# Performance work log

Measured on AMD Instinct MI355X. Metric: run time of the kernel, lower is better.

The kernel has to match this reference:

```python
import jax, jax.numpy as jnp
import numpy as np

L = 4        # num_blocks
D = 512      # d_model
H = 8        # num_heads
DFF = 2048   # d_ff
EPS = 1.1920929e-07  # torch RMSNorm default eps = finfo(fp32).eps


def setup_inputs() -> dict:
    key = jax.random.key(0)
    ks = jax.random.split(key, 12)
    B, S = 4, 1024
    s = 0.02
    return {
        "x": jax.random.normal(ks[0], (B, S, D), jnp.float32),
        "col_ids": jax.random.randint(ks[1], (B, S), 0, 32),
        "row_ids": jax.random.randint(ks[2], (B, S), 0, 128),
        "nbr_ids": jax.random.randint(ks[3], (B, S), 0, 64),
        # per-block, per-relation attention weights (nn.Linear: y = x @ W.T)
        "Wq": jax.random.normal(ks[4], (L, 4, D, D), jnp.float32) * s,
        "Wk": jax.random.normal(ks[5], (L, 4, D, D), jnp.float32) * s,
        "Wv": jax.random.normal(ks[6], (L, 4, D, D), jnp.float32) * s,
        "Wo": jax.random.normal(ks[7], (L, 4, D, D), jnp.float32) * s,
        # SwiGLU FFN weights per block
        "W1": jax.random.normal(ks[8], (L, DFF, D), jnp.float32) * s,
        "W3": jax.random.normal(ks[9], (L, DFF, D), jnp.float32) * s,
        "W2": jax.random.normal(ks[10], (L, D, DFF), jnp.float32) * s,
        # RMSNorm scales: 4 attn norms + 1 ffn norm per block + final norm_out
        "g_attn": jnp.ones((L, 4, D), jnp.float32),
        "g_ffn": jnp.ones((L, D), jnp.float32),
        "g_out": jnp.ones((D,), jnp.float32),
    }


def _rms(x, g):
    return x * jax.lax.rsqrt(jnp.mean(x * x, axis=-1, keepdims=True) + EPS) * g


def _attn(x, wq, wk, wv, wo, mask):
    # x: [B,S,D]; mask: [B,S,S] bool (True = attend) or None for full attention
    B, S, _ = x.shape
    hd = D // H
    scale = 1.0 / np.sqrt(hd).astype(np.float32)
    q = (x @ wq.T).reshape(B, S, H, hd).transpose(0, 2, 1, 3)  # bhsd
    k = (x @ wk.T).reshape(B, S, H, hd).transpose(0, 2, 1, 3)
    v = (x @ wv.T).reshape(B, S, H, hd).transpose(0, 2, 1, 3)
    sc = jnp.einsum('bhqd,bhkd->bhqk', q, k) * scale
    if mask is not None:
        sc = jnp.where(mask[:, None, :, :], sc, jnp.float32(-1e30))
    a = jax.nn.softmax(sc, axis=-1)
    o = jnp.einsum('bhqk,bhkd->bhqd', a, v).transpose(0, 2, 1, 3).reshape(B, S, D)
    return o @ wo.T


def reference(x, col_ids, row_ids, nbr_ids, Wq, Wk, Wv, Wo, W1, W3, W2, g_attn, g_ffn, g_out):
    # relation order in RelationalBlock: col, feat, nbr, full
    masks = [ids[:, :, None] == ids[:, None, :] for ids in (col_ids, row_ids, nbr_ids)] + [None]
    for l in range(L):
        for r in range(4):
            x = x + _attn(_rms(x, g_attn[l, r]), Wq[l, r], Wk[l, r], Wv[l, r], Wo[l, r], masks[r])
        h = _rms(x, g_ffn[l])
        x = x + (jax.nn.silu(h @ W1[l].T) * (h @ W3[l].T)) @ W2[l].T
    return _rms(x, g_out)
```

## Files before the change

kernel.cpp:

```cpp
#include <hip/hip_runtime.h>
#include <hip/hip_bf16.h>


typedef __attribute__((ext_vector_type(4))) float f32x4;
typedef __attribute__((ext_vector_type(8))) short s16x8;
typedef __attribute__((ext_vector_type(4))) short s16x4;

#define SEQ 1024
#define DM 512
#define MTOT 4096
#define EPSV 1.1920929e-07f
#define LOG2E 1.44269504088896f

static __device__ __forceinline__ float b2f(short s) {
  unsigned u = ((unsigned)(unsigned short)s) << 16;
  return __builtin_bit_cast(float, u);
}
static __device__ __forceinline__ short f2b(float f) {
  unsigned u = __builtin_bit_cast(unsigned, f);
  u = (u + 0x7fffu + ((u >> 16) & 1u)) >> 16;
  return (short)(unsigned short)u;
}

#define MFMA_BF16(a, b, c) __builtin_amdgcn_mfma_f32_16x16x32_bf16((a), (b), (c), 0, 0, 0)
#define GLLDS(gp, lp)                                                                        \
  __builtin_amdgcn_global_load_lds((const __attribute__((address_space(1))) unsigned*)(gp),  \
                                   (__attribute__((address_space(3))) unsigned*)(lp), 16, 0, 0)
#define GLLDS4(gp, lp)                                                                       \
  __builtin_amdgcn_global_load_lds((const __attribute__((address_space(1))) unsigned*)(gp),  \
                                   (__attribute__((address_space(3))) unsigned*)(lp), 4, 0, 0)

__global__ void cvt_place(const f32x4* __restrict__ src, s16x4* __restrict__ dst, int n4,
                          int shift, int stride4, int off4, float scale) {
  int i = blockIdx.x * 256 + threadIdx.x;
  if (i >= n4) return;
  f32x4 v = src[i];
  s16x4 o;
  o[0] = f2b(v[0] * scale); o[1] = f2b(v[1] * scale);
  o[2] = f2b(v[2] * scale); o[3] = f2b(v[3] * scale);
  int c = i >> shift, r = i & ((1 << shift) - 1);
  dst[(size_t)c * stride4 + off4 + r] = o;
}

__global__ void cvt_w13(const f32x4* __restrict__ src, s16x4* __restrict__ dst, int n4, int off) {
  int i = blockIdx.x * 256 + threadIdx.x;
  if (i >= n4) return;
  f32x4 v = src[i];
  s16x4 o;
  o[0] = f2b(v[0]); o[1] = f2b(v[1]); o[2] = f2b(v[2]); o[3] = f2b(v[3]);
  int srcrow = i >> 7, r = i & 127;
  int l = srcrow >> 11, n = srcrow & 2047;
  int dstrow = l * 4096 + n * 2 + off;
  dst[(size_t)dstrow * 128 + r] = o;
}

template<bool F32OUT>
__global__ void rmsnorm_kernel(const float* __restrict__ x, const float* __restrict__ g,
                               void* __restrict__ outp) {
  int row = blockIdx.x * 4 + (threadIdx.x >> 6);
  int lane = threadIdx.x & 63;
  const float* xr = x + (size_t)row * DM + lane * 8;
  f32x4 a = *(const f32x4*)xr;
  f32x4 b = *(const f32x4*)(xr + 4);
  float ss = a[0]*a[0]+a[1]*a[1]+a[2]*a[2]+a[3]*a[3]+b[0]*b[0]+b[1]*b[1]+b[2]*b[2]+b[3]*b[3];
#pragma unroll
  for (int m = 1; m < 64; m <<= 1) ss += __shfl_xor(ss, m, 64);
  float sc = rsqrtf(ss * (1.0f / DM) + EPSV);
  const float* gp = g + lane * 8;
  if (F32OUT) {
    float* o = (float*)outp + (size_t)row * DM + lane * 8;
    f32x4 o0, o1;
#pragma unroll
    for (int j = 0; j < 4; j++) { o0[j] = a[j] * sc * gp[j]; o1[j] = b[j] * sc * gp[4 + j]; }
    *(f32x4*)o = o0;
    *(f32x4*)(o + 4) = o1;
  } else {
    s16x8 o;
#pragma unroll
    for (int j = 0; j < 4; j++) { o[j] = f2b(a[j] * sc * gp[j]); o[4 + j] = f2b(b[j] * sc * gp[4 + j]); }
    *(s16x8*)((short*)outp + (size_t)row * DM + lane * 8) = o;
  }
}

template<int AR, int AC, int FUSE>
__global__ __launch_bounds__(256) void gemm_bt(const short* __restrict__ A, const short* __restrict__ W,
                                               short* __restrict__ outb, float* __restrict__ outf,
                                               short* __restrict__ vtb, int N, int K) {
  constexpr int BM = AR * 32;
  constexpr int BN = AC * 32;
  constexpr int LPS = BM / 64 + BN / 64;
  __shared__ short As[2][BM * 32];
  __shared__ short Bs[2][BN * 32];
  const int tid = threadIdx.x;
  const int lane = tid & 63;
  const int w = tid >> 6;
  const int wr = w >> 1, wc = w & 1;
  const int m0 = blockIdx.x * BM, n0 = blockIdx.y * BN;
  f32x4 acc[AR][AC] = {};

#define STAGE_GEMM(buf, kk)                                                                      \
  {                                                                                              \
    _Pragma("unroll")                                                                            \
    for (int i = 0; i < BM / 64; i++) {                                                          \
      int s = i * 256 + tid;                                                                     \
      int row = s >> 2, gl = s & 3, gd = gl ^ ((row >> 1) & 3);                                  \
      GLLDS(A + (size_t)(m0 + row) * K + (kk) + gd * 8, (char*)As[buf] + (i * 256 + w * 64) * 16);\
    }                                                                                            \
    _Pragma("unroll")                                                                            \
    for (int i = 0; i < BN / 64; i++) {                                                          \
      int s = i * 256 + tid;                                                                     \
      int row = s >> 2, gl = s & 3, gd = gl ^ ((row >> 1) & 3);                                  \
      GLLDS(W + (size_t)(n0 + row) * K + (kk) + gd * 8, (char*)Bs[buf] + (i * 256 + w * 64) * 16);\
    }                                                                                            \
  }

  STAGE_GEMM(0, 0);
  STAGE_GEMM(1, 32);
  asm volatile("s_waitcnt vmcnt(%0)" :: "n"(LPS) : "memory");
  __builtin_amdgcn_s_barrier();
  int cur = 0;
  const int nt = K >> 5;
  for (int t = 0; t < nt; ++t) {
    s16x8 af[AR], bf[AC];
#pragma unroll
    for (int i = 0; i < AR; i++) {
      int row = wr * AR * 16 + i * 16 + (lane & 15);
      int gl = (lane >> 4) ^ ((row >> 1) & 3);
      af[i] = *(const s16x8*)(As[cur] + row * 32 + gl * 8);
    }
#pragma unroll
    for (int j = 0; j < AC; j++) {
      int row = wc * AC * 16 + j * 16 + (lane & 15);
      int gl = (lane >> 4) ^ ((row >> 1) & 3);
      bf[j] = *(const s16x8*)(Bs[cur] + row * 32 + gl * 8);
    }
    asm volatile("s_waitcnt lgkmcnt(0)" ::: "memory");
    __builtin_amdgcn_s_barrier();
    if (t + 2 < nt) STAGE_GEMM(cur, (t + 2) * 32);
#pragma unroll
    for (int i = 0; i < AR; i++)
#pragma unroll
      for (int j = 0; j < AC; j++)
        acc[i][j] = MFMA_BF16(af[i], bf[j], acc[i][j]);
    if (t + 2 < nt) asm volatile("s_waitcnt vmcnt(%0)" :: "n"(LPS) : "memory");
    else            asm volatile("s_waitcnt vmcnt(0)" ::: "memory");
    __builtin_amdgcn_s_barrier();
    cur ^= 1;
  }
#undef STAGE_GEMM

#pragma unroll
  for (int i = 0; i < AR; i++) {
    int rbase = m0 + wr * AR * 16 + i * 16 + (lane >> 4) * 4;
#pragma unroll
    for (int j = 0; j < AC; j++) {
      int col = n0 + wc * AC * 16 + j * 16 + (lane & 15);
      if (FUSE == 2 && col >= 1024) {
        int bbv = rbase >> 10, s = rbase & 1023;
        int c = col - 1024, hhv = c >> 6, d = c & 63;
        int o = (s & 63) >> 2;
        int gg = o & 3, h2 = (o >> 2) & 1, q32 = o >> 3;
        int pnew = q32 * 8 + gg * 2 + h2;
        s16x4 o4;
#pragma unroll
        for (int r = 0; r < 4; r++) o4[r] = f2b(acc[i][j][r]);
        *(s16x4*)(vtb + (((size_t)(bbv * 8 + hhv) * 64 + d) << 10) + (s & ~63) + pnew * 4) = o4;
      } else if (FUSE == 3) {
#pragma unroll
        for (int r = 0; r < 4; r++) {
          float own = acc[i][j][r];
          float other = __shfl_xor(own, 1, 64);
          float sv = own / (1.0f + __expf(-own));
          if (!(lane & 1))
            outb[(size_t)(rbase + r) * (N >> 1) + (col >> 1)] = f2b(sv * other);
        }
      } else {
#pragma unroll
        for (int r = 0; r < 4; r++) {
          size_t idx = (size_t)(rbase + r) * N + col;
          if (FUSE == 1) outf[idx] += acc[i][j][r];
          else           outb[idx] = f2b(acc[i][j][r]);
        }
      }
    }
  }
}

__global__ __launch_bounds__(256) void attn_kernel(const short* __restrict__ qkv, const short* __restrict__ vt,
                                                   const int* __restrict__ ids, short* __restrict__ Ob) {
  const int bh = blockIdx.x;
  const int bb = bh >> 3, hh = bh & 7;
  const int q0 = blockIdx.y * 64;
  const int tid = threadIdx.x, lane = tid & 63, w = tid >> 6;
  const int g = lane >> 4, qi = lane & 15;
  __shared__ short Kl[2][128 * 64];
  __shared__ short Vl[2][64 * 128];
  __shared__ int Kid[2][128];
  const short* kbase = qkv + 512 + hh * 64;
  const short* vbase = vt + (size_t)bh * 64 * SEQ;
  s16x8 qf0, qf1;
  {
    int qrow = q0 + w * 16 + qi;
    const short* qp = qkv + (size_t)(bb * SEQ + qrow) * 1536 + hh * 64 + g * 8;
    qf0 = *(const s16x8*)qp;
    qf1 = *(const s16x8*)(qp + 32);
  }
  int qid = 0;
  if (ids) qid = ids[bb * SEQ + q0 + w * 16 + qi];
  float m_ = -1e30f, l_ = 0.f;
  f32x4 oacc[4] = {};

#define STAGE_ATTN(buf, ktt)                                                                     \
  {                                                                                              \
    _Pragma("unroll")                                                                            \
    for (int i = 0; i < 4; i++) {                                                                \
      int s = i * 256 + tid;                                                                     \
      int row = s >> 3, gl = s & 7, gd = gl ^ (row & 7);                                         \
      GLLDS(kbase + (size_t)(bb * SEQ + (ktt) + row) * 1536 + gd * 8,                            \
            (char*)Kl[buf] + (i * 256 + w * 64) * 16);                                           \
    }                                                                                            \
    _Pragma("unroll")                                                                            \
    for (int i = 0; i < 4; i++) {                                                                \
      int s = i * 256 + tid;                                                                     \
      int d = s >> 4, gl = s & 15, gd = gl ^ (d & 7);                                            \
      GLLDS(vbase + (size_t)d * SEQ + (ktt) + gd * 8, (char*)Vl[buf] + (i * 256 + w * 64) * 16); \
    }                                                                                            \
    if (ids && w < 2) GLLDS4(ids + bb * SEQ + (ktt) + w * 64 + lane, (char*)Kid[buf] + w * 256); \
  }

  STAGE_ATTN(0, 0);
  __syncthreads();
  int cur = 0;
  for (int kt = 0; kt < SEQ; kt += 128) {
    if (kt + 128 < SEQ) STAGE_ATTN(cur ^ 1, kt + 128);
    f32x4 sc[8];
#pragma unroll
    for (int kc = 0; kc < 8; kc++) {
      int krow = kc * 16 + qi;
      s16x8 kf0 = *(const s16x8*)(Kl[cur] + krow * 64 + ((g ^ (krow & 7)) * 8));
      s16x8 kf1 = *(const s16x8*)(Kl[cur] + krow * 64 + (((4 + g) ^ (krow & 7)) * 8));
      f32x4 s4 = {};
      s4 = MFMA_BF16(kf0, qf0, s4);
      s4 = MFMA_BF16(kf1, qf1, s4);
      sc[kc] = s4;
    }
    float p[8][4];
#pragma unroll
    for (int kc = 0; kc < 8; kc++)
#pragma unroll
      for (int r = 0; r < 4; r++) p[kc][r] = sc[kc][r];
    if (ids) {
#pragma unroll
      for (int kc = 0; kc < 8; kc++) {
        int4 kid4 = *(const int4*)(Kid[cur] + kc * 16 + g * 4);
        if (kid4.x != qid) p[kc][0] = -1e30f;
        if (kid4.y != qid) p[kc][1] = -1e30f;
        if (kid4.z != qid) p[kc][2] = -1e30f;
        if (kid4.w != qid) p[kc][3] = -1e30f;
      }
    }
    float mx = fmaxf(fmaxf(p[0][0], p[0][1]), fmaxf(p[0][2], p[0][3]));
#pragma unroll
    for (int kc = 1; kc < 8; kc++)
      mx = fmaxf(mx, fmaxf(fmaxf(p[kc][0], p[kc][1]), fmaxf(p[kc][2], p[kc][3])));
    mx = fmaxf(mx, __shfl_xor(mx, 16, 64));
    mx = fmaxf(mx, __shfl_xor(mx, 32, 64));
    if (__any(mx > m_ + 8.f)) {
      float nm = fmaxf(m_, mx);
      float c = exp2f(m_ - nm);
      m_ = nm;
      l_ *= c;
#pragma unroll
      for (int r = 0; r < 4; r++) {
        float cr = __shfl(c, g * 4 + r, 16);
        oacc[0][r] *= cr; oacc[1][r] *= cr; oacc[2][r] *= cr; oacc[3][r] *= cr;
      }
    }
    float sum = 0.f;
#pragma unroll
    for (int kc = 0; kc < 8; kc++)
#pragma unroll
      for (int r = 0; r < 4; r++) {
        p[kc][r] = exp2f(p[kc][r] - m_);
        sum += p[kc][r];
      }
    sum += __shfl_xor(sum, 16, 64);
    sum += __shfl_xor(sum, 32, 64);
    l_ += sum;
#pragma unroll
    for (int kk = 0; kk < 2; kk++) {
      s16x8 pa, pb;
#pragma unroll
      for (int r = 0; r < 4; r++) {
        pa[r] = f2b(p[kk * 4 + 0][r]); pa[4 + r] = f2b(p[kk * 4 + 1][r]);
        pb[r] = f2b(p[kk * 4 + 2][r]); pb[4 + r] = f2b(p[kk * 4 + 3][r]);
      }
#pragma unroll
      for (int dt = 0; dt < 4; dt++) {
        int dl = dt * 16 + qi;
        const short* vr = Vl[cur] + dl * 128;
        s16x8 vf0 = *(const s16x8*)(vr + (kk * 8 + (g ^ (dl & 7))) * 8);
        s16x8 vf1 = *(const s16x8*)(vr + (kk * 8 + ((4 + g) ^ (dl & 7))) * 8);
        oacc[dt] = MFMA_BF16(pa, vf0, oacc[dt]);
        oacc[dt] = MFMA_BF16(pb, vf1, oacc[dt]);
      }
    }
    __syncthreads();
    cur ^= 1;
  }
#undef STAGE_ATTN
  const size_t obase = (size_t)(bb * SEQ) * DM + hh * 64;
#pragma unroll
  for (int r = 0; r < 4; r++) {
    float lr = __shfl(l_, g * 4 + r, 16);
    float inv = 1.0f / lr;
    int q = q0 + w * 16 + g * 4 + r;
#pragma unroll
    for (int dt = 0; dt < 4; dt++)
      Ob[obase + (size_t)q * DM + dt * 16 + qi] = f2b(oacc[dt][r] * inv);
  }
}

extern "C" void kernel_launch(void* const* d_in, const int* in_sizes, int n_in,
                              void* d_out, int out_size, void* d_ws, size_t ws_size,
                              hipStream_t stream) {
  const float* x_in  = (const float*)d_in[0];
  const int* col_ids = (const int*)d_in[1];
  const int* row_ids = (const int*)d_in[2];
  const int* nbr_ids = (const int*)d_in[3];
  const float* g_attn = (const float*)d_in[11];
  const float* g_ffn  = (const float*)d_in[12];
  const float* g_out  = (const float*)d_in[13];

  char* ws = (char*)d_ws;
  float* x   = (float*)(ws);
  short* h   = (short*)(ws + (size_t)(8u  << 20));
  short* qkv = (short*)(ws + (size_t)(12u << 20));
  short* vt  = (short*)(ws + (size_t)(24u << 20));
  short* ob  = (short*)(ws + (size_t)(28u << 20));
  short* fa  = (short*)(ws + (size_t)(44u << 20));
  short* wqkv = (short*)(ws + (size_t)(60u  << 20));
  short* wob  = (short*)(ws + (size_t)(84u  << 20));
  short* w13  = (short*)(ws + (size_t)(92u  << 20));
  short* w2b  = (short*)(ws + (size_t)(108u << 20));

  const int N4 = 1048576;
  cvt_place<<<4096, 256, 0, stream>>>((const f32x4*)d_in[4], (s16x4*)wqkv, N4, 16, 196608, 0, 0.125f * LOG2E);
  cvt_place<<<4096, 256, 0, stream>>>((const f32x4*)d_in[5], (s16x4*)wqkv, N4, 16, 196608, 65536, 1.0f);
  cvt_place<<<4096, 256, 0, stream>>>((const f32x4*)d_in[6], (s16x4*)wqkv, N4, 16, 196608, 131072, 1.0f);
  cvt_place<<<4096, 256, 0, stream>>>((const f32x4*)d_in[7], (s16x4*)wob,  N4, 20, 0, 0, 1.0f);
  cvt_w13<<<4096, 256, 0, stream>>>((const f32x4*)d_in[8], (s16x4*)w13, N4, 0);
  cvt_w13<<<4096, 256, 0, stream>>>((const f32x4*)d_in[9], (s16x4*)w13, N4, 1);
  cvt_place<<<4096, 256, 0, stream>>>((const f32x4*)d_in[10], (s16x4*)w2b, N4, 20, 0, 0, 1.0f);

  hipMemcpyAsync(x, x_in, (size_t)MTOT * DM * 4, hipMemcpyDeviceToDevice, stream);

  const int* idsarr[4] = {col_ids, row_ids, nbr_ids, nullptr};

  for (int l = 0; l < 4; l++) {
    for (int r = 0; r < 4; r++) {
      rmsnorm_kernel<false><<<1024, 256, 0, stream>>>(x, g_attn + (size_t)(l * 4 + r) * DM, (void*)h);
      size_t woff = (size_t)(l * 4 + r) * 1536 * DM;
      gemm_bt<4, 4, 2><<<dim3(32, 12), 256, 0, stream>>>(h, wqkv + woff, qkv, nullptr, vt, 1536, DM);
      attn_kernel<<<dim3(32, 16), 256, 0, stream>>>(qkv, vt, idsarr[r], ob);
      gemm_bt<2, 2, 1><<<dim3(64, 8), 256, 0, stream>>>(ob, wob + (size_t)(l * 4 + r) * DM * DM,
                                                        nullptr, x, nullptr, DM, DM);
    }
    rmsnorm_kernel<false><<<1024, 256, 0, stream>>>(x, g_ffn + (size_t)l * DM, (void*)h);
    gemm_bt<4, 4, 3><<<dim3(32, 32), 256, 0, stream>>>(h, w13 + (size_t)l * 4096 * DM, fa, nullptr, nullptr, 4096, DM);
    gemm_bt<2, 2, 1><<<dim3(64, 8), 256, 0, stream>>>(fa, w2b + (size_t)l * DM * 2048, nullptr, x, nullptr, DM, 2048);
  }
  rmsnorm_kernel<true><<<1024, 256, 0, stream>>>(x, g_out, d_out);
}
```

Before: 1.171 ms.

## Hoist GEMM address math, unroll K-loop by two, shrink QKV/FFN1 N-tiles

The GEMM kernel now computes global load pointers and swizzled LDS read offsets once before the loop and advances the pointers by 32 elements per stage. The K loop is manually unrolled by two so the double-buffer index is a compile-time constant. Separately, the QKV and W1/W3 GEMMs switch from 128x128 to 128x64 tiles, doubling the grid for more blocks per CU. The smaller tiles reduce per-tile reuse and raise global/L2 traffic for the A operand. The unroll assumes an even K-tile count, which holds for K=512 and 2048.

```diff
diff --git a/kernel.cpp b/kernel.cpp
--- a/kernel.cpp
+++ b/kernel.cpp
@@ -88,73 +88,97 @@
                                                short* __restrict__ vtb, int N, int K) {
   constexpr int BM = AR * 32;
   constexpr int BN = AC * 32;
-  constexpr int LPS = BM / 64 + BN / 64;
+  constexpr int NA = BM / 64, NB = BN / 64;
+  constexpr int LPS = NA + NB;
   __shared__ short As[2][BM * 32];
   __shared__ short Bs[2][BN * 32];
   const int tid = threadIdx.x;
   const int lane = tid & 63;
   const int w = tid >> 6;
   const int wr = w >> 1, wc = w & 1;
+  const int qi = lane & 15, g = lane >> 4;
   const int m0 = blockIdx.x * BM, n0 = blockIdx.y * BN;
+
+  const short* ap[NA];
+  const short* wp[NB];
+#pragma unroll
+  for (int i = 0; i < NA; i++) {
+    int s = i * 256 + tid;
+    int row = s >> 2, gl = s & 3, gd = gl ^ ((row >> 1) & 3);
+    ap[i] = A + (size_t)(m0 + row) * K + gd * 8;
+  }
+#pragma unroll
+  for (int i = 0; i < NB; i++) {
+    int s = i * 256 + tid;
+    int row = s >> 2, gl = s & 3, gd = gl ^ ((row >> 1) & 3);
+    wp[i] = W + (size_t)(n0 + row) * K + gd * 8;
+  }
+  int aro[AR], bro[AC];
+#pragma unroll
+  for (int i = 0; i < AR; i++) {
+    int row = wr * AR * 16 + i * 16 + qi;
+    aro[i] = row * 64 + ((g ^ ((row >> 1) & 3)) * 16);
+  }
+#pragma unroll
+  for (int j = 0; j < AC; j++) {
+    int row = wc * AC * 16 + j * 16 + qi;
+    bro[j] = row * 64 + ((g ^ ((row >> 1) & 3)) * 16);
+  }
   f32x4 acc[AR][AC] = {};
 
-#define STAGE_GEMM(buf, kk)                                                                      \
-  {                                                                                              \
-    _Pragma("unroll")                                                                            \
-    for (int i = 0; i < BM / 64; i++) {                                                          \
-      int s = i * 256 + tid;                                                                     \
-      int row = s >> 2, gl = s & 3, gd = gl ^ ((row >> 1) & 3);                                  \
-      GLLDS(A + (size_t)(m0 + row) * K + (kk) + gd * 8, (char*)As[buf] + (i * 256 + w * 64) * 16);\
-    }                                                                                            \
-    _Pragma("unroll")                                                                            \
-    for (int i = 0; i < BN / 64; i++) {                                                          \
-      int s = i * 256 + tid;                                                                     \
-      int row = s >> 2, gl = s & 3, gd = gl ^ ((row >> 1) & 3);                                  \
-      GLLDS(W + (size_t)(n0 + row) * K + (kk) + gd * 8, (char*)Bs[buf] + (i * 256 + w * 64) * 16);\
-    }                                                                                            \
-  }
-
-  STAGE_GEMM(0, 0);
-  STAGE_GEMM(1, 32);
+#define STAGE_G(BUF)                                                             \
+  {                                                                              \
+    _Pragma("unroll")                                                            \
+    for (int i = 0; i < NA; i++) {                                               \
+      GLLDS(ap[i], (char*)As[BUF] + (i * 256 + w * 64) * 16);                    \
+      ap[i] += 32;                                                               \
+    }                                                                            \
+    _Pragma("unroll")                                                            \
+    for (int i = 0; i < NB; i++) {                                               \
+      GLLDS(wp[i], (char*)Bs[BUF] + (i * 256 + w * 64) * 16);                    \
+      wp[i] += 32;                                                               \
+    }                                                                            \
+  }
+
+#define BODY_G(BUF, T)                                                           \
+  {                                                                              \
+    s16x8 af[AR], bf[AC];                                                        \
+    _Pragma("unroll")                                                            \
+    for (int i = 0; i < AR; i++) af[i] = *(const s16x8*)((char*)As[BUF] + aro[i]); \
+    _Pragma("unroll")                                                            \
+    for (int j = 0; j < AC; j++) bf[j] = *(const s16x8*)((char*)Bs[BUF] + bro[j]); \
+    asm volatile("s_waitcnt lgkmcnt(0)" ::: "memory");                           \
+    __builtin_amdgcn_s_barrier();                                                \
+    bool more = ((T) + 2 < nt);                                                  \
+    if (more) STAGE_G(BUF);                                                      \
+    _Pragma("unroll")                                                            \
+    for (int i = 0; i < AR; i++)                                                 \
+      _Pragma("unroll")                                                          \
+      for (int j = 0; j < AC; j++)                                               \
+        acc[i][j] = MFMA_BF16(af[i], bf[j], acc[i][j]);                          \
+    if (more) asm volatile("s_waitcnt vmcnt(%0)" :: "n"(LPS) : "memory");        \
+    else      asm volatile("s_waitcnt vmcnt(0)" ::: "memory");                   \
+    __builtin_amdgcn_s_barrier();                                                \
+  }
+
+  const int nt = K >> 5;
+  STAGE_G(0);
+  STAGE_G(1);
   asm volatile("s_waitcnt vmcnt(%0)" :: "n"(LPS) : "memory");
   __builtin_amdgcn_s_barrier();
-  int cur = 0;
-  const int nt = K >> 5;
-  for (int t = 0; t < nt; ++t) {
-    s16x8 af[AR], bf[AC];
-#pragma unroll
-    for (int i = 0; i < AR; i++) {
-      int row = wr * AR * 16 + i * 16 + (lane & 15);
-      int gl = (lane >> 4) ^ ((row >> 1) & 3);
-      af[i] = *(const s16x8*)(As[cur] + row * 32 + gl * 8);
-    }
+  for (int t = 0; t < nt; t += 2) {
+    BODY_G(0, t);
+    BODY_G(1, t + 1);
+  }
+#undef STAGE_G
+#undef BODY_G
+
+#pragma unroll
+  for (int i = 0; i < AR; i++) {
+    int rbase = m0 + wr * AR * 16 + i * 16 + g * 4;
 #pragma unroll
     for (int j = 0; j < AC; j++) {
-      int row = wc * AC * 16 + j * 16 + (lane & 15);
-      int gl = (lane >> 4) ^ ((row >> 1) & 3);
-      bf[j] = *(const s16x8*)(Bs[cur] + row * 32 + gl * 8);
-    }
-    asm volatile("s_waitcnt lgkmcnt(0)" ::: "memory");
-    __builtin_amdgcn_s_barrier();
-    if (t + 2 < nt) STAGE_GEMM(cur, (t + 2) * 32);
-#pragma unroll
-    for (int i = 0; i < AR; i++)
-#pragma unroll
-      for (int j = 0; j < AC; j++)
-        acc[i][j] = MFMA_BF16(af[i], bf[j], acc[i][j]);
-    if (t + 2 < nt) asm volatile("s_waitcnt vmcnt(%0)" :: "n"(LPS) : "memory");
-    else            asm volatile("s_waitcnt vmcnt(0)" ::: "memory");
-    __builtin_amdgcn_s_barrier();
-    cur ^= 1;
-  }
-#undef STAGE_GEMM
-
-#pragma unroll
-  for (int i = 0; i < AR; i++) {
-    int rbase = m0 + wr * AR * 16 + i * 16 + (lane >> 4) * 4;
-#pragma unroll
-    for (int j = 0; j < AC; j++) {
-      int col = n0 + wc * AC * 16 + j * 16 + (lane & 15);
+      int col = n0 + wc * AC * 16 + j * 16 + qi;
       if (FUSE == 2 && col >= 1024) {
         int bbv = rbase >> 10, s = rbase & 1023;
         int c = col - 1024, hhv = c >> 6, d = c & 63;
@@ -361,13 +385,13 @@
     for (int r = 0; r < 4; r++) {
       rmsnorm_kernel<false><<<1024, 256, 0, stream>>>(x, g_attn + (size_t)(l * 4 + r) * DM, (void*)h);
       size_t woff = (size_t)(l * 4 + r) * 1536 * DM;
-      gemm_bt<4, 4, 2><<<dim3(32, 12), 256, 0, stream>>>(h, wqkv + woff, qkv, nullptr, vt, 1536, DM);
+      gemm_bt<4, 2, 2><<<dim3(32, 24), 256, 0, stream>>>(h, wqkv + woff, qkv, nullptr, vt, 1536, DM);
       attn_kernel<<<dim3(32, 16), 256, 0, stream>>>(qkv, vt, idsarr[r], ob);
       gemm_bt<2, 2, 1><<<dim3(64, 8), 256, 0, stream>>>(ob, wob + (size_t)(l * 4 + r) * DM * DM,
                                                         nullptr, x, nullptr, DM, DM);
     }
     rmsnorm_kernel<false><<<1024, 256, 0, stream>>>(x, g_ffn + (size_t)l * DM, (void*)h);
-    gemm_bt<4, 4, 3><<<dim3(32, 32), 256, 0, stream>>>(h, w13 + (size_t)l * 4096 * DM, fa, nullptr, nullptr, 4096, DM);
+    gemm_bt<4, 2, 3><<<dim3(32, 64), 256, 0, stream>>>(h, w13 + (size_t)l * 4096 * DM, fa, nullptr, nullptr, 4096, DM);
     gemm_bt<2, 2, 1><<<dim3(64, 8), 256, 0, stream>>>(fa, w2b + (size_t)l * DM * 2048, nullptr, x, nullptr, DM, 2048);
   }
   rmsnorm_kernel<true><<<1024, 256, 0, stream>>>(x, g_out, d_out);
```

Measured after the change: 1.139 ms. 1.03x faster.
